# Kernel optimization log

Measured on AMD Instinct MI355X. Metric: run time of the kernel, lower is better.

## Reference

```python
import jax, jax.numpy as jnp
import numpy as np

EPS = 1e-5


def _layernorm(x, w, b):
    mu = jnp.mean(x, axis=-1, keepdims=True)
    var = jnp.var(x, axis=-1, keepdims=True)
    return (x - mu) * jax.lax.rsqrt(var + EPS) * w + b


def setup_inputs() -> dict:
    key = jax.random.key(0)
    ks = jax.random.split(key, 5)
    B, I, H = 8192, 1024, 1024
    inp = {
        "input": jax.random.normal(ks[0], (B, I), dtype=jnp.float32),
        "hx": jax.random.normal(ks[1], (B, H), dtype=jnp.float32),
        "cx": jax.random.normal(ks[2], (B, H), dtype=jnp.float32),
        # parameters (torch initializes weights with randn; LN weight=1, bias=0)
        "weight_ih": jax.random.normal(ks[3], (4 * H, I), dtype=jnp.float32),
        "weight_hh": jax.random.normal(ks[4], (4 * H, H), dtype=jnp.float32),
        "ln_i_w": jnp.ones((4 * H,), jnp.float32),
        "ln_i_b": jnp.zeros((4 * H,), jnp.float32),
        "ln_h_w": jnp.ones((4 * H,), jnp.float32),
        "ln_h_b": jnp.zeros((4 * H,), jnp.float32),
        "ln_c_w": jnp.ones((H,), jnp.float32),
        "ln_c_b": jnp.zeros((H,), jnp.float32),
    }
    return inp


def reference(input, hx, cx, weight_ih, weight_hh,
              ln_i_w, ln_i_b, ln_h_w, ln_h_b, ln_c_w, ln_c_b):
    # gate pre-activations: [B, 4H]
    igates = _layernorm(input @ weight_ih.T, ln_i_w, ln_i_b)
    hgates = _layernorm(hx @ weight_hh.T, ln_h_w, ln_h_b)
    gates = igates + hgates
    ingate, forgetgate, cellgate, outgate = jnp.split(gates, 4, axis=-1)
    ingate = jax.nn.sigmoid(ingate)
    forgetgate = jax.nn.sigmoid(forgetgate)
    cellgate = jnp.tanh(cellgate)
    outgate = jax.nn.sigmoid(outgate)
    cy = _layernorm(forgetgate * cx + ingate * cellgate, ln_c_w, ln_c_b)
    hy = outgate * jnp.tanh(cy)  # activation=Tanh, dropout p=0 is identity
    return (hy, cy)
```

## Files before the change

kernel.cpp:

```cpp
#include <hip/hip_runtime.h>
#include <hip/hip_bf16.h>
#include <cstdint>
#include <cstddef>

typedef __bf16 bf16_t;
typedef bf16_t bf16x8 __attribute__((ext_vector_type(8)));
typedef bf16_t bf16x4v __attribute__((ext_vector_type(4)));
typedef float floatx4 __attribute__((ext_vector_type(4)));

static constexpr int B_ = 8192;
static constexpr int H_ = 1024;
static constexpr int G4 = 4096;
static constexpr int K_ = 1024;

__device__ inline void async_copy16(const bf16_t* g, bf16_t* l) {
  auto l3 = (__attribute__((address_space(3))) void*)(uint32_t)(uintptr_t)l;
  __builtin_amdgcn_global_load_lds(
      (__attribute__((address_space(1))) void*)(uintptr_t)g, l3, 16, 0, 0);
}

__global__ __launch_bounds__(256) void cast2_f32_bf16(
    const float* __restrict__ a, const float* __restrict__ b,
    bf16_t* __restrict__ oa, bf16_t* __restrict__ ob, int n8each) {
  int gid = blockIdx.x * blockDim.x + threadIdx.x;
  const float* src; bf16_t* dst; int idx;
  if (gid < n8each) { src = a; dst = oa; idx = gid; }
  else              { src = b; dst = ob; idx = gid - n8each; }
  const float4 v0 = ((const float4*)src)[idx * 2];
  const float4 v1 = ((const float4*)src)[idx * 2 + 1];
  bf16x8 o;
  o[0] = (bf16_t)v0.x; o[1] = (bf16_t)v0.y; o[2] = (bf16_t)v0.z; o[3] = (bf16_t)v0.w;
  o[4] = (bf16_t)v1.x; o[5] = (bf16_t)v1.y; o[6] = (bf16_t)v1.z; o[7] = (bf16_t)v1.w;
  ((bf16x8*)dst)[idx] = o;
}

__global__ __launch_bounds__(256) void cast_w_perm(
    const float* __restrict__ wih, const float* __restrict__ whh,
    bf16_t* __restrict__ oih, bf16_t* __restrict__ ohh) {
  const int rp = blockIdx.x & 4095;
  const float* src = (blockIdx.x < 4096) ? wih : whh;
  bf16_t*      dst = (blockIdx.x < 4096) ? oih : ohh;
  const int h = rp >> 2, g = rp & 3;
  const int rin = g * 1024 + h;
  const int c = threadIdx.x * 4;
  const float4 v = *(const float4*)(src + (size_t)rin * K_ + c);
  bf16x4v o;
  o[0] = (bf16_t)v.x; o[1] = (bf16_t)v.y; o[2] = (bf16_t)v.z; o[3] = (bf16_t)v.w;
  *(bf16x4v*)(dst + (size_t)rp * K_ + c) = o;
}

__global__ __launch_bounds__(256) void gemm_bt_dual(
    const bf16_t* __restrict__ A0, const bf16_t* __restrict__ A1,
    const bf16_t* __restrict__ W0, const bf16_t* __restrict__ W1,
    bf16_t* __restrict__ C0, bf16_t* __restrict__ C1) {
  constexpr int N = G4, K = K_;
  const bf16_t* A = blockIdx.z ? A1 : A0;
  const bf16_t* W = blockIdx.z ? W1 : W0;
  bf16_t*       C = blockIdx.z ? C1 : C0;

  __shared__ bf16_t As[128 * 32];
  __shared__ bf16_t Bs[128 * 32];

  const int tid  = threadIdx.x;
  const int lane = tid & 63;
  const int wid  = tid >> 6;
  const int wm   = wid >> 1, wn = wid & 1;
  const int lrow = lane & 15, quad = lane >> 4;

  const int m0 = blockIdx.y * 128;
  const int n0 = blockIdx.x * 128;

  const int L0 = tid;
  const int L1 = 256 + tid;
  const int c0 = (((L0 & 3) ^ ((L0 >> 3) & 3))) * 8;
  const int c1 = (((L1 & 3) ^ ((L1 >> 3) & 3))) * 8;
  const bf16_t* gA0 = A + (size_t)(m0 + (L0 >> 2)) * K + c0;
  const bf16_t* gA1 = A + (size_t)(m0 + (L1 >> 2)) * K + c1;
  const bf16_t* gB0 = W + (size_t)(n0 + (L0 >> 2)) * K + c0;
  const bf16_t* gB1 = W + (size_t)(n0 + (L1 >> 2)) * K + c1;
  bf16_t* lA0 = As + wid * 512;
  bf16_t* lA1 = As + 2048 + wid * 512;
  bf16_t* lB0 = Bs + wid * 512;
  bf16_t* lB1 = Bs + 2048 + wid * 512;

  const int qc = (quad ^ ((lrow >> 1) & 3)) * 8;

  floatx4 acc[4][4] = {};

  for (int k0 = 0; k0 < K; k0 += 32) {
    __syncthreads();
    async_copy16(gA0 + k0, lA0);
    async_copy16(gA1 + k0, lA1);
    async_copy16(gB0 + k0, lB0);
    async_copy16(gB1 + k0, lB1);
    __syncthreads();

    bf16x8 af[4], bfr[4];
#pragma unroll
    for (int i = 0; i < 4; ++i)
      af[i] = *(const bf16x8*)&As[(wm * 64 + i * 16 + lrow) * 32 + qc];
#pragma unroll
    for (int j = 0; j < 4; ++j)
      bfr[j] = *(const bf16x8*)&Bs[(wn * 64 + j * 16 + lrow) * 32 + qc];
#pragma unroll
    for (int i = 0; i < 4; ++i)
#pragma unroll
      for (int j = 0; j < 4; ++j)
        acc[i][j] = __builtin_amdgcn_mfma_f32_16x16x32_bf16(af[i], bfr[j],
                                                            acc[i][j], 0, 0, 0);
  }

#pragma unroll
  for (int i = 0; i < 4; ++i) {
    const int mbase = m0 + wm * 64 + i * 16 + quad * 4;
#pragma unroll
    for (int j = 0; j < 4; ++j) {
      const int n = n0 + wn * 64 + j * 16 + lrow;
#pragma unroll
      for (int r = 0; r < 4; ++r)
        C[(size_t)(mbase + r) * N + n] = (bf16_t)acc[i][j][r];
    }
  }
}

__device__ inline float sigmoid_f(float x) { return 1.0f / (1.0f + __expf(-x)); }
__device__ inline float tanh_f(float x) {
  float e = __expf(2.0f * x);
  return 1.0f - 2.0f / (e + 1.0f);
}

__global__ __launch_bounds__(256) void ln_lstm_epilogue(
    const bf16_t* __restrict__ IG, const bf16_t* __restrict__ HG,
    const float* __restrict__ cx,
    const float* __restrict__ wi, const float* __restrict__ bi,
    const float* __restrict__ wh, const float* __restrict__ bh,
    const float* __restrict__ wc, const float* __restrict__ bc,
    float* __restrict__ hy_out, float* __restrict__ cy_out) {
  const int b = blockIdx.x;
  const int t = threadIdx.x;
  const int lane = t & 63;
  const int wid = t >> 6;

  __shared__ float red1[4][4];
  __shared__ float red2[4][2];

  const bf16x8 ig0 = *(const bf16x8*)(IG + (size_t)b * 4096 + t * 16);
  const bf16x8 ig1 = *(const bf16x8*)(IG + (size_t)b * 4096 + t * 16 + 8);
  const bf16x8 hg0 = *(const bf16x8*)(HG + (size_t)b * 4096 + t * 16);
  const bf16x8 hg1 = *(const bf16x8*)(HG + (size_t)b * 4096 + t * 16 + 8);
  const float4 cx4 = *(const float4*)(cx + (size_t)b * 1024 + t * 4);

  float vi[16], vh[16];
#pragma unroll
  for (int e = 0; e < 8; ++e) {
    vi[e] = (float)ig0[e]; vi[8 + e] = (float)ig1[e];
    vh[e] = (float)hg0[e]; vh[8 + e] = (float)hg1[e];
  }
  float si = 0, qi = 0, sh = 0, qh = 0;
#pragma unroll
  for (int k = 0; k < 16; ++k) {
    si += vi[k]; qi = fmaf(vi[k], vi[k], qi);
    sh += vh[k]; qh = fmaf(vh[k], vh[k], qh);
  }
#pragma unroll
  for (int off = 32; off; off >>= 1) {
    si += __shfl_down(si, off); qi += __shfl_down(qi, off);
    sh += __shfl_down(sh, off); qh += __shfl_down(qh, off);
  }
  if (lane == 0) { red1[wid][0] = si; red1[wid][1] = qi; red1[wid][2] = sh; red1[wid][3] = qh; }
  __syncthreads();
  si = red1[0][0] + red1[1][0] + red1[2][0] + red1[3][0];
  qi = red1[0][1] + red1[1][1] + red1[2][1] + red1[3][1];
  sh = red1[0][2] + red1[1][2] + red1[2][2] + red1[3][2];
  qh = red1[0][3] + red1[1][3] + red1[2][3] + red1[3][3];

  const float invN = 1.0f / 4096.0f;
  const float mui = si * invN, muh = sh * invN;
  const float rsi = rsqrtf(fmaxf(qi * invN - mui * mui, 0.0f) + 1e-5f);
  const float rsh = rsqrtf(fmaxf(qh * invN - muh * muh, 0.0f) + 1e-5f);

  float4 wig[4], big[4], whg[4], bhg[4];
#pragma unroll
  for (int g = 0; g < 4; ++g) {
    wig[g] = *(const float4*)(wi + g * 1024 + t * 4);
    big[g] = *(const float4*)(bi + g * 1024 + t * 4);
    whg[g] = *(const float4*)(wh + g * 1024 + t * 4);
    bhg[g] = *(const float4*)(bh + g * 1024 + t * 4);
  }

  const float cxa[4] = {cx4.x, cx4.y, cx4.z, cx4.w};
  float cv[4], ov[4];
  float sc = 0, qc2 = 0;
#pragma unroll
  for (int j = 0; j < 4; ++j) {
    const float wg[4] = {((const float*)&wig[0])[j], ((const float*)&wig[1])[j],
                         ((const float*)&wig[2])[j], ((const float*)&wig[3])[j]};
    const float bg[4] = {((const float*)&big[0])[j], ((const float*)&big[1])[j],
                         ((const float*)&big[2])[j], ((const float*)&big[3])[j]};
    const float wg2[4] = {((const float*)&whg[0])[j], ((const float*)&whg[1])[j],
                          ((const float*)&whg[2])[j], ((const float*)&whg[3])[j]};
    const float bg2[4] = {((const float*)&bhg[0])[j], ((const float*)&bhg[1])[j],
                          ((const float*)&bhg[2])[j], ((const float*)&bhg[3])[j]};
    float G[4];
#pragma unroll
    for (int g = 0; g < 4; ++g) {
      const int e = j * 4 + g;
      G[g] = (vi[e] - mui) * rsi * wg[g] + bg[g] +
             (vh[e] - muh) * rsh * wg2[g] + bg2[g];
    }
    const float in_g = sigmoid_f(G[0]);
    const float fo_g = sigmoid_f(G[1]);
    const float ce_g = tanh_f(G[2]);
    ov[j] = sigmoid_f(G[3]);
    const float c = fo_g * cxa[j] + in_g * ce_g;
    cv[j] = c;
    sc += c; qc2 = fmaf(c, c, qc2);
  }
#pragma unroll
  for (int off = 32; off; off >>= 1) {
    sc += __shfl_down(sc, off); qc2 += __shfl_down(qc2, off);
  }
  if (lane == 0) { red2[wid][0] = sc; red2[wid][1] = qc2; }
  __syncthreads();
  sc = red2[0][0] + red2[1][0] + red2[2][0] + red2[3][0];
  qc2 = red2[0][1] + red2[1][1] + red2[2][1] + red2[3][1];
  const float invH = 1.0f / 1024.0f;
  const float muc = sc * invH;
  const float rsc = rsqrtf(fmaxf(qc2 * invH - muc * muc, 0.0f) + 1e-5f);

  const float4 wc4 = ((const float4*)wc)[t];
  const float4 bc4 = ((const float4*)bc)[t];
  const float wca[4] = {wc4.x, wc4.y, wc4.z, wc4.w};
  const float bca[4] = {bc4.x, bc4.y, bc4.z, bc4.w};
  float4 hyv, cyv;
#pragma unroll
  for (int j = 0; j < 4; ++j) {
    const float cyn = (cv[j] - muc) * rsc * wca[j] + bca[j];
    ((float*)&cyv)[j] = cyn;
    ((float*)&hyv)[j] = ov[j] * tanh_f(cyn);
  }
  *(float4*)(cy_out + (size_t)b * 1024 + t * 4) = cyv;
  *(float4*)(hy_out + (size_t)b * 1024 + t * 4) = hyv;
}

extern "C" void kernel_launch(void* const* d_in, const int* in_sizes, int n_in,
                              void* d_out, int out_size, void* d_ws, size_t ws_size,
                              hipStream_t stream) {
  const float* input  = (const float*)d_in[0];
  const float* hx     = (const float*)d_in[1];
  const float* cx     = (const float*)d_in[2];
  const float* w_ih   = (const float*)d_in[3];
  const float* w_hh   = (const float*)d_in[4];
  const float* ln_i_w = (const float*)d_in[5];
  const float* ln_i_b = (const float*)d_in[6];
  const float* ln_h_w = (const float*)d_in[7];
  const float* ln_h_b = (const float*)d_in[8];
  const float* ln_c_w = (const float*)d_in[9];
  const float* ln_c_b = (const float*)d_in[10];

  float* out = (float*)d_out;
  float* hy = out;
  float* cy = out + (size_t)B_ * H_;

  bf16_t* Abf = (bf16_t*)d_ws;
  bf16_t* Hbf = Abf + (size_t)B_ * K_;
  bf16_t* Wib = Hbf + (size_t)B_ * K_;
  bf16_t* Whb = Wib + (size_t)G4 * K_;
  bf16_t* IG  = Whb + (size_t)G4 * K_;
  bf16_t* HG  = IG + (size_t)B_ * G4;

  const int n8 = B_ * K_ / 8;
  cast2_f32_bf16<<<(2 * n8) / 256, 256, 0, stream>>>(input, hx, Abf, Hbf, n8);
  cast_w_perm<<<2 * G4, 256, 0, stream>>>(w_ih, w_hh, Wib, Whb);

  gemm_bt_dual<<<dim3(G4 / 128, B_ / 128, 2), 256, 0, stream>>>(Abf, Hbf, Wib, Whb, IG, HG);

  ln_lstm_epilogue<<<B_, 256, 0, stream>>>(IG, HG, cx, ln_i_w, ln_i_b,
                                           ln_h_w, ln_h_b, ln_c_w, ln_c_b, hy, cy);
}
```

Baseline: 381.4 us.

## Replace GEMM with 256x256 double-buffered 8-wave pipelined MFMA kernel

Replaces the 128x128, single-buffered, 4-wave bf16 GEMM with a 256x256 tile, 512-thread kernel that uses K=64 steps and double-buffered LDS. Global-to-LDS async loads for the next tiles are interleaved with four MFMA quadrant phases, with explicit waitcnt, sched_barrier and setprio control. The larger tiles increase data reuse and the pipelining hides load latency behind MFMAs. In exchange it uses 128KB of LDS per block, many barriers, and hand-tuned vmcnt counts, and the wraparound prefetch loads redundant data on the last iterations.

After: 363.2 us. -4.8%, faster.

```diff
diff --git a/kernel.cpp b/kernel.cpp
--- a/kernel.cpp
+++ b/kernel.cpp
@@ -49,70 +49,122 @@
   *(bf16x4v*)(dst + (size_t)rp * K_ + c) = o;
 }
 
-__global__ __launch_bounds__(256) void gemm_bt_dual(
+
+#define FENCE() asm volatile("" ::: "memory")
+#define BARRIER() do { FENCE(); __builtin_amdgcn_s_barrier(); FENCE(); } while (0)
+
+__global__ __launch_bounds__(512, 2) void gemm_bt_dual8(
     const bf16_t* __restrict__ A0, const bf16_t* __restrict__ A1,
     const bf16_t* __restrict__ W0, const bf16_t* __restrict__ W1,
     bf16_t* __restrict__ C0, bf16_t* __restrict__ C1) {
-  constexpr int N = G4, K = K_;
+  constexpr int N = G4, K = K_, NT = K_ / 64;
+
+  __shared__ bf16_t ldsA[2][16384];
+  __shared__ bf16_t ldsB[2][16384];
+
   const bf16_t* A = blockIdx.z ? A1 : A0;
   const bf16_t* W = blockIdx.z ? W1 : W0;
   bf16_t*       C = blockIdx.z ? C1 : C0;
 
-  __shared__ bf16_t As[128 * 32];
-  __shared__ bf16_t Bs[128 * 32];
-
   const int tid  = threadIdx.x;
   const int lane = tid & 63;
-  const int wid  = tid >> 6;
-  const int wm   = wid >> 1, wn = wid & 1;
+  const int w    = tid >> 6;
+  const int wm   = w >> 2, wn = w & 3;
   const int lrow = lane & 15, quad = lane >> 4;
-
-  const int m0 = blockIdx.y * 128;
-  const int n0 = blockIdx.x * 128;
-
-  const int L0 = tid;
-  const int L1 = 256 + tid;
-  const int c0 = (((L0 & 3) ^ ((L0 >> 3) & 3))) * 8;
-  const int c1 = (((L1 & 3) ^ ((L1 >> 3) & 3))) * 8;
-  const bf16_t* gA0 = A + (size_t)(m0 + (L0 >> 2)) * K + c0;
-  const bf16_t* gA1 = A + (size_t)(m0 + (L1 >> 2)) * K + c1;
-  const bf16_t* gB0 = W + (size_t)(n0 + (L0 >> 2)) * K + c0;
-  const bf16_t* gB1 = W + (size_t)(n0 + (L1 >> 2)) * K + c1;
-  bf16_t* lA0 = As + wid * 512;
-  bf16_t* lA1 = As + 2048 + wid * 512;
-  bf16_t* lB0 = Bs + wid * 512;
-  bf16_t* lB1 = Bs + 2048 + wid * 512;
-
-  const int qc = (quad ^ ((lrow >> 1) & 3)) * 8;
-
-  floatx4 acc[4][4] = {};
-
-  for (int k0 = 0; k0 < K; k0 += 32) {
-    __syncthreads();
-    async_copy16(gA0 + k0, lA0);
-    async_copy16(gA1 + k0, lA1);
-    async_copy16(gB0 + k0, lB0);
-    async_copy16(gB1 + k0, lB1);
-    __syncthreads();
-
-    bf16x8 af[4], bfr[4];
-#pragma unroll
-    for (int i = 0; i < 4; ++i)
-      af[i] = *(const bf16x8*)&As[(wm * 64 + i * 16 + lrow) * 32 + qc];
-#pragma unroll
-    for (int j = 0; j < 4; ++j)
-      bfr[j] = *(const bf16x8*)&Bs[(wn * 64 + j * 16 + lrow) * 32 + qc];
-#pragma unroll
-    for (int i = 0; i < 4; ++i)
-#pragma unroll
-      for (int j = 0; j < 4; ++j)
-        acc[i][j] = __builtin_amdgcn_mfma_f32_16x16x32_bf16(af[i], bfr[j],
-                                                            acc[i][j], 0, 0, 0);
-  }
-
-#pragma unroll
-  for (int i = 0; i < 4; ++i) {
-    const int mbase = m0 + wm * 64 + i * 16 + quad * 4;
+  const int e    = lrow & 7;
+
+  const int m0 = blockIdx.y * 256;
+  const int n0 = blockIdx.x * 256;
+
+  const int srow   = tid >> 3;
+  const int schunk = (tid & 7) ^ (srow & 7);
+  const bf16_t* gA = A + (size_t)(m0 + srow) * K + schunk * 8;
+  const bf16_t* gB = W + (size_t)(n0 + srow) * K + schunk * 8;
+  const int wslot = w * 512;
+
+  const int aBase = (wm * 128 + lrow) * 64 + (quad ^ e) * 8;
+  const int bBase = (wn * 64 + lrow) * 64 + (quad ^ e) * 8;
+
+  floatx4 acc[8][4] = {};
+  bf16x8 aF[4][2];
+  bf16x8 bF[2][2][2];
+
+#define STG_A(p, half, kt) do {                                          \
+    bf16_t* _l = &ldsA[p][(half) * 8192 + wslot];                        \
+    async_copy16(gA + (size_t)((half) * 128) * K + (kt) * 64, _l);       \
+    async_copy16(gA + (size_t)((half) * 128 + 64) * K + (kt) * 64, _l + 4096); \
+  } while (0)
+#define STG_B(p, half, kt) do {                                          \
+    bf16_t* _l = &ldsB[p][(half) * 8192 + wslot];                        \
+    async_copy16(gB + (size_t)((half) * 128) * K + (kt) * 64, _l);       \
+    async_copy16(gB + (size_t)((half) * 128 + 64) * K + (kt) * 64, _l + 4096); \
+  } while (0)
+
+#define LD_A(p, qm) do { _Pragma("unroll")                               \
+    for (int i2 = 0; i2 < 4; ++i2) {                                     \
+      const int o = aBase + (qm) * 4096 + i2 * 1024;                     \
+      aF[i2][0] = *(const bf16x8*)&ldsA[p][o];                           \
+      aF[i2][1] = *(const bf16x8*)&ldsA[p][o ^ 32];                      \
+    } } while (0)
+#define LD_B(p, qn) do { _Pragma("unroll")                               \
+    for (int j2 = 0; j2 < 2; ++j2) {                                     \
+      const int o = bBase + (qn) * 2048 + j2 * 1024;                     \
+      bF[qn][j2][0] = *(const bf16x8*)&ldsB[p][o];                       \
+      bF[qn][j2][1] = *(const bf16x8*)&ldsB[p][o ^ 32];                  \
+    } } while (0)
+#define MFMA_Q(qm, qn) do { _Pragma("unroll")                            \
+    for (int i2 = 0; i2 < 4; ++i2) { _Pragma("unroll")                   \
+      for (int j2 = 0; j2 < 2; ++j2) {                                   \
+        floatx4& c = acc[(qm) * 4 + i2][(qn) * 2 + j2];                  \
+        c = __builtin_amdgcn_mfma_f32_16x16x32_bf16(aF[i2][0], bF[qn][j2][0], c, 0, 0, 0); \
+        c = __builtin_amdgcn_mfma_f32_16x16x32_bf16(aF[i2][1], bF[qn][j2][1], c, 0, 0, 0); \
+      } } } while (0)
+
+  STG_B(0, 0, 0); STG_B(0, 1, 0);
+  STG_A(0, 0, 0); STG_A(0, 1, 0);
+  STG_B(1, 0, 1); STG_B(1, 1, 1);
+  asm volatile("s_waitcnt vmcnt(4)" ::: "memory");
+  BARRIER();
+
+#pragma unroll 2
+  for (int t = 0; t < NT; ++t) {
+    const int p = t & 1, q = p ^ 1;
+    const int t1 = (t + 1) & (NT - 1), t2 = (t + 2) & (NT - 1);
+
+    LD_A(p, 0); LD_B(p, 0);
+    STG_A(q, 0, t1);
+    BARRIER();
+    asm volatile("s_waitcnt lgkmcnt(0)" ::: "memory");
+    __builtin_amdgcn_sched_barrier(0);
+    __builtin_amdgcn_s_setprio(1); MFMA_Q(0, 0); __builtin_amdgcn_s_setprio(0);
+    BARRIER();
+
+    LD_B(p, 1);
+    STG_A(q, 1, t1);
+    BARRIER();
+    asm volatile("s_waitcnt lgkmcnt(0)" ::: "memory");
+    __builtin_amdgcn_sched_barrier(0);
+    __builtin_amdgcn_s_setprio(1); MFMA_Q(0, 1); __builtin_amdgcn_s_setprio(0);
+    BARRIER();
+
+    LD_A(p, 1);
+    STG_B(p, 0, t2);
+    BARRIER();
+    asm volatile("s_waitcnt lgkmcnt(0)" ::: "memory");
+    __builtin_amdgcn_sched_barrier(0);
+    __builtin_amdgcn_s_setprio(1); MFMA_Q(1, 0); __builtin_amdgcn_s_setprio(0);
+    BARRIER();
+
+    STG_B(p, 1, t2);
+    BARRIER();
+    __builtin_amdgcn_s_setprio(1); MFMA_Q(1, 1); __builtin_amdgcn_s_setprio(0);
+    asm volatile("s_waitcnt vmcnt(4)" ::: "memory");
+    BARRIER();
+  }
+
+#pragma unroll
+  for (int i = 0; i < 8; ++i) {
+    const int mbase = m0 + wm * 128 + i * 16 + quad * 4;
 #pragma unroll
     for (int j = 0; j < 4; ++j) {
       const int n = n0 + wn * 64 + j * 16 + lrow;
@@ -121,6 +173,11 @@
         C[(size_t)(mbase + r) * N + n] = (bf16_t)acc[i][j][r];
     }
   }
+#undef STG_A
+#undef STG_B
+#undef LD_A
+#undef LD_B
+#undef MFMA_Q
 }
 
 __device__ inline float sigmoid_f(float x) { return 1.0f / (1.0f + __expf(-x)); }
@@ -273,7 +330,7 @@
   cast2_f32_bf16<<<(2 * n8) / 256, 256, 0, stream>>>(input, hx, Abf, Hbf, n8);
   cast_w_perm<<<2 * G4, 256, 0, stream>>>(w_ih, w_hh, Wib, Whb);
 
-  gemm_bt_dual<<<dim3(G4 / 128, B_ / 128, 2), 256, 0, stream>>>(Abf, Hbf, Wib, Whb, IG, HG);
+  gemm_bt_dual8<<<dim3(G4 / 256, B_ / 256, 2), 512, 0, stream>>>(Abf, Hbf, Wib, Whb, IG, HG);
 
   ln_lstm_epilogue<<<B_, 256, 0, stream>>>(IG, HG, cx, ln_i_w, ln_i_b,
                                            ln_h_w, ln_h_b, ln_c_w, ln_c_b, hy, cy);
```
